# Optimization experiments

Measured on AMD Instinct MI355X. Metric: run time of the kernel, lower is better.

## Reference

```python
import jax, jax.numpy as jnp
import numpy as np


def setup_inputs() -> dict:
    key = jax.random.key(0)
    ks = jax.random.split(key, 5)
    B, S, C = 512, 512, 96
    emissions = jax.random.normal(ks[0], (B, S, C), dtype=jnp.float32)
    tags = jax.random.randint(ks[1], (B, S), 0, C, dtype=jnp.int64)
    masks = jnp.ones((B, S), dtype=bool)
    start_transitions = jax.random.uniform(ks[2], (C,), jnp.float32, -0.1, 0.1)
    end_transitions = jax.random.uniform(ks[3], (C,), jnp.float32, -0.1, 0.1)
    transitions = jax.random.uniform(ks[4], (C, C), jnp.float32, -0.1, 0.1)
    return {
        "emissions": emissions,
        "tags": tags,
        "masks": masks,
        "start_transitions": start_transitions,
        "end_transitions": end_transitions,
        "transitions": transitions,
    }


def _crf_llh(emissions, tags, masks, start_transitions, end_transitions, transitions):
    # to time-major: (S, B, C), (S, B)
    emissions = jnp.swapaxes(emissions, 0, 1)
    tags = jnp.swapaxes(tags, 0, 1)
    masks = jnp.swapaxes(masks, 0, 1)
    S, B, C = emissions.shape
    maskf = masks.astype(emissions.dtype)

    # ---- numerator: score of the gold tag path (fully vectorized over time) ----
    em_scores = jnp.take_along_axis(emissions, tags[:, :, None], axis=2)[:, :, 0]  # (S, B)
    trans_scores = transitions[tags[:-1], tags[1:]]  # (S-1, B)
    score = start_transitions[tags[0]] + em_scores[0]
    score = score + jnp.sum((trans_scores + em_scores[1:]) * maskf[1:], axis=0)
    seq_ends = masks.astype(jnp.int32).sum(axis=0) - 1  # (B,)
    last_tags = tags[seq_ends, jnp.arange(B)]
    numerator = score + end_transitions[last_tags]

    # ---- denominator: forward algorithm (sequential logsumexp recurrence) ----
    alpha0 = start_transitions[None, :] + emissions[0]  # (B, C)

    def step(alpha, inp):
        em_i, m_i = inp  # (B, C), (B,)
        # (B, C_prev, C_next)
        scores = alpha[:, :, None] + transitions[None, :, :] + em_i[:, None, :]
        next_alpha = jax.scipy.special.logsumexp(scores, axis=1)
        alpha = jnp.where(m_i[:, None], next_alpha, alpha)
        return alpha, None

    alpha, _ = jax.lax.scan(step, alpha0, (emissions[1:], masks[1:]))
    denominator = jax.scipy.special.logsumexp(alpha + end_transitions[None, :], axis=1)

    return jnp.mean(numerator - denominator)


def reference(emissions, tags, masks, start_transitions, end_transitions, transitions):
    return _crf_llh(emissions, tags, masks, start_transitions, end_transitions, transitions)
```

## Files before the change

### kernel.cpp

```cpp
#include <hip/hip_runtime.h>
#include <hip/hip_bf16.h>
#include <math.h>


#define BATCH 512
#define SEQ   512
#define NC    96
#define NTHR  128
#define LN2   0.69314718055994531f

typedef __fp16 half2v __attribute__((ext_vector_type(2)));

#define BARRIER() asm volatile("s_waitcnt lgkmcnt(0)\n\ts_barrier" ::: "memory")

#define DPP_STEP_F(v, op, ctrl)                                              \
    v = op(v, __int_as_float(__builtin_amdgcn_update_dpp(                    \
            __float_as_int(v), __float_as_int(v), (ctrl), 0xf, 0xf, false)))

__device__ __forceinline__ float wave_max_all(float v) {
    DPP_STEP_F(v, fmaxf, 0x111);
    DPP_STEP_F(v, fmaxf, 0x112);
    DPP_STEP_F(v, fmaxf, 0x114);
    DPP_STEP_F(v, fmaxf, 0x118);
    DPP_STEP_F(v, fmaxf, 0x142);
    DPP_STEP_F(v, fmaxf, 0x143);
    return __int_as_float(__builtin_amdgcn_readlane(__float_as_int(v), 63));
}
__device__ __forceinline__ float fadd_(float a, float b) { return a + b; }
__device__ __forceinline__ float wave_sum_all(float v) {
    DPP_STEP_F(v, fadd_, 0x111);
    DPP_STEP_F(v, fadd_, 0x112);
    DPP_STEP_F(v, fadd_, 0x114);
    DPP_STEP_F(v, fadd_, 0x118);
    DPP_STEP_F(v, fadd_, 0x142);
    DPP_STEP_F(v, fadd_, 0x143);
    return __int_as_float(__builtin_amdgcn_readlane(__float_as_int(v), 63));
}

__global__ __launch_bounds__(NTHR, 1)
void crf_llh_kernel(const float* __restrict__ em,
                    const int*   __restrict__ tags,
                    const int*   __restrict__ masks,
                    const float* __restrict__ startT,
                    const float* __restrict__ endT,
                    const float* __restrict__ trans,
                    float*       __restrict__ out)
{
    const int b    = blockIdx.x;
    const int tid  = threadIdx.x;
    const int lane = tid & 63;
    const int wid  = tid >> 6;
    const bool active = (tid < NC);
    const int jc = active ? tid : 0;

    __shared__ __align__(16) __fp16 qsh[2][128];
    __shared__ float maxsh[2][2];
    __shared__ float redn[2], redm[2], redd[2];

    const float* em_b    = em    + (size_t)b * SEQ * NC;
    const int*   tags_b  = tags  + b * SEQ;
    const int*   masks_b = masks + b * SEQ;

    half2v ecol[48];
    #pragma unroll
    for (int k = 0; k < 48; ++k) {
        ecol[k] = __builtin_amdgcn_cvt_pkrtz(
            __expf(trans[(2 * k)     * NC + jc]),
            __expf(trans[(2 * k + 1) * NC + jc]));
    }

    const float al0 = startT[jc] + em_b[jc];
    {
        const float wm = wave_max_all(active ? al0 : -1e30f);
        if (lane == 0) maxsh[0][wid] = wm;
    }
    BARRIER();
    const float M0 = fmaxf(maxsh[0][0], maxsh[0][1]);
    float wreg = active ? __expf(al0 - M0) : 0.f;
    qsh[1][tid] = (__fp16)wreg;
    BARRIER();

    int K    = 1;
    int sumk = 0;

    float emA = em_b[1 * NC + jc];
    float emB = em_b[2 * NC + jc];
    float emC = em_b[3 * NC + jc];
    int mkA = masks_b[1], mkB = masks_b[2], mkC = masks_b[3];

    for (int s = 1; s < SEQ; ++s) {
        const int rb = s & 1;
        const int sp = (s + 3 < SEQ) ? (s + 3) : (SEQ - 1);
        const float emN = em_b[sp * NC + jc];
        const int   mkN = masks_b[sp];

        const uint4* q4p = reinterpret_cast<const uint4*>(&qsh[rb][0]);
        uint4 qv[12];
        #pragma unroll
        for (int t = 0; t < 12; ++t) qv[t] = q4p[t];

        float acc[6] = {0.f, 0.f, 0.f, 0.f, 0.f, 0.f};
        #pragma unroll
        for (int t = 0; t < 12; ++t) {
            const half2v qx = __builtin_bit_cast(half2v, qv[t].x);
            const half2v qy = __builtin_bit_cast(half2v, qv[t].y);
            const half2v qz = __builtin_bit_cast(half2v, qv[t].z);
            const half2v qw = __builtin_bit_cast(half2v, qv[t].w);
            acc[(4 * t + 0) % 6] = __builtin_amdgcn_fdot2(qx, ecol[4 * t + 0], acc[(4 * t + 0) % 6], false);
            acc[(4 * t + 1) % 6] = __builtin_amdgcn_fdot2(qy, ecol[4 * t + 1], acc[(4 * t + 1) % 6], false);
            acc[(4 * t + 2) % 6] = __builtin_amdgcn_fdot2(qz, ecol[4 * t + 2], acc[(4 * t + 2) % 6], false);
            acc[(4 * t + 3) % 6] = __builtin_amdgcn_fdot2(qw, ecol[4 * t + 3], acc[(4 * t + 3) % 6], false);
        }
        const float U = ((acc[0] + acc[1]) + (acc[2] + acc[3])) + (acc[4] + acc[5]);

        const float F = __expf(emA);
        float w = ldexpf(U, -(K + 6)) * F;
        if (!active) w = 0.f;
        w = mkA ? w : wreg;
        sumk += mkA ? (K + 6) : 0;
        wreg = w;

        const float wmx = wave_max_all(w);
        if (lane == 0) maxsh[rb][wid] = wmx;
        qsh[rb ^ 1][tid] = (__fp16)w;
        BARRIER();

        const float r = fmaxf(maxsh[rb][0], maxsh[rb][1]);
        K = (int)((__float_as_uint(r) >> 23) & 255u) - 126;

        emA = emB; emB = emC; emC = emN;
        mkA = mkB; mkB = mkC; mkC = mkN;
    }

    const float dv = active ? wreg * __expf(endT[jc]) : 0.f;
    {
        const float ws = wave_sum_all(dv);
        if (lane == 0) redd[wid] = ws;
    }
    __syncthreads();
    const float denom = M0 + (float)sumk * LN2 + __logf(redd[0] + redd[1]);

    float nsum = 0.f, msum = 0.f;
    #pragma unroll
    for (int kk = 0; kk < SEQ / NTHR; ++kk) {
        const int s  = tid + NTHR * kk;
        const int tg = tags_b[s];
        const int mk = masks_b[s];
        msum += mk ? 1.f : 0.f;
        if (s == 0) {
            nsum += startT[tg] + em_b[tg];
        } else if (mk) {
            nsum += trans[tags_b[s - 1] * NC + tg] + em_b[s * NC + tg];
        }
    }
    nsum = wave_sum_all(nsum);
    msum = wave_sum_all(msum);
    if (lane == 0) { redn[wid] = nsum; redm[wid] = msum; }
    __syncthreads();
    if (tid == 0) {
        const float numer = redn[0] + redn[1];
        const int   cnt   = (int)(redm[0] + redm[1]);
        const int   last  = tags_b[cnt - 1];
        atomicAdd(out, (numer + endT[last] - denom) * (1.0f / (float)BATCH));
    }
}

extern "C" void kernel_launch(void* const* d_in, const int* in_sizes, int n_in,
                              void* d_out, int out_size, void* d_ws, size_t ws_size,
                              hipStream_t stream) {
    const float* em     = (const float*)d_in[0];
    const int*   tags   = (const int*)  d_in[1];
    const int*   masks  = (const int*)  d_in[2];
    const float* startT = (const float*)d_in[3];
    const float* endT   = (const float*)d_in[4];
    const float* trans  = (const float*)d_in[5];
    float* out = (float*)d_out;

    (void)hipMemsetAsync(out, 0, sizeof(float), stream);
    crf_llh_kernel<<<BATCH, NTHR, 0, stream>>>(em, tags, masks, startT, endT, trans, out);
}
```

Baseline: 402.9 us.

## Batch 16 sequences per block and run forward recurrence on MFMA

The forward-algorithm recurrence now handles 16 batch rows per block, so each step becomes a 16x96 by 96x96 fp16 matrix product on MFMA instructions instead of per-thread fdot2 loops. A second wave acts as a producer that prefetches emissions, exponentiates them to fp16 and stages them in a 16-slot shared ring, so one barrier covers every four steps. Rescaling uses per-row power-of-two exponents. The numerator moves to a separate kernel. This cuts the grid to 32 blocks, which lowers occupancy, and adds fp16 rounding risk and a second launch.

New measurement: 581.2 us. 44.3% more time.

```diff
diff --git a/kernel.cpp b/kernel.cpp
--- a/kernel.cpp
+++ b/kernel.cpp
@@ -1,15 +1,21 @@
 #include <hip/hip_runtime.h>
-#include <hip/hip_bf16.h>
 #include <math.h>
 
 
 #define BATCH 512
 #define SEQ   512
 #define NC    96
+#define CH    16
+#define NBLK  (BATCH/CH)
 #define NTHR  128
 #define LN2   0.69314718055994531f
+#define FPAT  0x0001000100010001ull
 
 typedef __fp16 half2v __attribute__((ext_vector_type(2)));
+typedef __fp16 half8  __attribute__((ext_vector_type(8)));
+typedef float  f32x4  __attribute__((ext_vector_type(4)));
+typedef unsigned int uint2v __attribute__((ext_vector_type(2)));
+typedef unsigned int uint4v __attribute__((ext_vector_type(4)));
 
 #define BARRIER() asm volatile("s_waitcnt lgkmcnt(0)\n\ts_barrier" ::: "memory")
 
@@ -36,110 +42,311 @@
     DPP_STEP_F(v, fadd_, 0x143);
     return __int_as_float(__builtin_amdgcn_readlane(__float_as_int(v), 63));
 }
+__device__ __forceinline__ float grp16_max(float v) {
+    DPP_STEP_F(v, fmaxf, 0xB1);
+    DPP_STEP_F(v, fmaxf, 0x4E);
+    DPP_STEP_F(v, fmaxf, 0x141);
+    DPP_STEP_F(v, fmaxf, 0x140);
+    return v;
+}
+__device__ __forceinline__ unsigned pk_rtn(float a, float b) {
+    half2v h; h[0] = (__fp16)a; h[1] = (__fp16)b;
+    return __builtin_bit_cast(unsigned, h);
+}
+__device__ __forceinline__ float dot8(half8 a, uint4v b, float c) {
+    uint4v au = __builtin_bit_cast(uint4v, a);
+    c = __builtin_amdgcn_fdot2(__builtin_bit_cast(half2v, au.x), __builtin_bit_cast(half2v, b.x), c, false);
+    c = __builtin_amdgcn_fdot2(__builtin_bit_cast(half2v, au.y), __builtin_bit_cast(half2v, b.y), c, false);
+    c = __builtin_amdgcn_fdot2(__builtin_bit_cast(half2v, au.z), __builtin_bit_cast(half2v, b.z), c, false);
+    c = __builtin_amdgcn_fdot2(__builtin_bit_cast(half2v, au.w), __builtin_bit_cast(half2v, b.w), c, false);
+    return c;
+}
 
 __global__ __launch_bounds__(NTHR, 1)
-void crf_llh_kernel(const float* __restrict__ em,
-                    const int*   __restrict__ tags,
-                    const int*   __restrict__ masks,
-                    const float* __restrict__ startT,
-                    const float* __restrict__ endT,
-                    const float* __restrict__ trans,
-                    float*       __restrict__ out)
+void crf_denom_kernel(const float* __restrict__ em,
+                      const int*   __restrict__ masks,
+                      const float* __restrict__ startT,
+                      const float* __restrict__ endT,
+                      const float* __restrict__ trans,
+                      float*       __restrict__ out)
+{
+    const int tid = threadIdx.x;
+    const int l   = tid & 63;
+    const int w   = tid >> 6;
+    const int c0  = blockIdx.x * CH;
+    const int grp = l >> 4;
+    const int lid = l & 15;
+
+    __shared__ __align__(16) __fp16 Wl[NC * CH];
+    __shared__ __align__(16) __fp16 EMR[16][CH * 104];
+    __shared__ __align__(8)  unsigned short FLG[16][CH];
+    __shared__ __align__(16) __fp16 ENDX[NC];
+    __shared__ int SKC[CH];
+
+    if (w == 0) {
+        float Ms;
+        {
+            float a = startT[l];
+            float b = (l < 32) ? startT[64 + l] : -1e30f;
+            Ms = wave_max_all(fmaxf(a, b));
+        }
+        if (l < 48)
+            ((unsigned*)ENDX)[l] = pk_rtn(__expf(endT[2 * l]), __expf(endT[2 * l + 1]));
+        #pragma unroll
+        for (int t = 0; t < 12; ++t) {
+            const int di = t * 64 + l;
+            const int k  = di >> 3;
+            const float v0 = __expf(startT[k] - Ms);
+            ((unsigned*)Wl)[di] = pk_rtn(v0, v0);
+        }
+        half8 Eb[3][6];
+        #pragma unroll
+        for (int t = 0; t < 3; ++t)
+            #pragma unroll
+            for (int nt = 0; nt < 6; ++nt) {
+                half8 bv;
+                #pragma unroll
+                for (int j = 0; j < 8; ++j)
+                    bv[j] = (__fp16)__expf(trans[(32 * t + grp * 8 + j) * NC + nt * 16 + lid]);
+                Eb[t][nt] = bv;
+            }
+
+        const unsigned wtr = (unsigned)(unsigned long long)Wl + (unsigned)(grp * 256);
+        char* const wpc    = (char*)Wl + lid * 32 + grp * 8;
+        const int   emoff  = lid * 104 + grp * 8;
+
+        half8 ap0{}, ap1{}, ap2{};
+        float m0 = 1.f, m1 = 1.f, m2 = 1.f, m3 = 1.f;
+        float scl0 = 1.f, scl1 = 1.f, scl2 = 1.f, scl3 = 1.f;
+        int   ks0 = 0, ks1 = 0, ks2 = 0, ks3 = 0;
+        int   sk0 = 0, sk1 = 0, sk2 = 0, sk3 = 0;
+
+        #pragma unroll 1
+        for (int s = 1; s <= SEQ - 1; ++s) {
+            if ((s & 3) == 1) BARRIER();
+            const int slotc = (s - 1) & 15;
+            const unsigned long long fqp =
+                *(const unsigned long long*)(&FLG[slotc][grp * 4]);
+            uint2v t0, t1, t2, t3, t4, t5;
+            asm volatile("ds_read_b64_tr_b16 %0, %1"             : "=v"(t0) : "v"(wtr) : "memory");
+            asm volatile("ds_read_b64_tr_b16 %0, %1 offset:128"  : "=v"(t1) : "v"(wtr) : "memory");
+            asm volatile("ds_read_b64_tr_b16 %0, %1 offset:1024" : "=v"(t2) : "v"(wtr) : "memory");
+            asm volatile("ds_read_b64_tr_b16 %0, %1 offset:1152" : "=v"(t3) : "v"(wtr) : "memory");
+            asm volatile("ds_read_b64_tr_b16 %0, %1 offset:2048" : "=v"(t4) : "v"(wtr) : "memory");
+            asm volatile("ds_read_b64_tr_b16 %0, %1 offset:2176" : "=v"(t5) : "v"(wtr) : "memory");
+            const __fp16* emp = &EMR[slotc][0] + emoff;
+            const uint4v e0 = *(const uint4v*)(emp);
+            const uint4v e1 = *(const uint4v*)(emp + 32);
+            const uint4v e2 = *(const uint4v*)(emp + 64);
+            const int allp = __all(fqp == FPAT);
+
+            m0 = grp16_max(m0); m1 = grp16_max(m1);
+            m2 = grp16_max(m2); m3 = grp16_max(m3);
+            const unsigned eb0 = (__float_as_uint(m0) >> 23) & 255u;
+            const unsigned eb1 = (__float_as_uint(m1) >> 23) & 255u;
+            const unsigned eb2 = (__float_as_uint(m2) >> 23) & 255u;
+            const unsigned eb3 = (__float_as_uint(m3) >> 23) & 255u;
+            if (allp) {
+                sk0 += ks0; sk1 += ks1; sk2 += ks2; sk3 += ks3;
+                ks0 = (int)eb0 - 120; ks1 = (int)eb1 - 120;
+                ks2 = (int)eb2 - 120; ks3 = (int)eb3 - 120;
+                scl0 = __uint_as_float((247u - eb0) << 23);
+                scl1 = __uint_as_float((247u - eb1) << 23);
+                scl2 = __uint_as_float((247u - eb2) << 23);
+                scl3 = __uint_as_float((247u - eb3) << 23);
+            } else {
+                if ((unsigned)(fqp      ) & 1u) { sk0 += ks0; ks0 = (int)eb0 - 120; scl0 = __uint_as_float((247u - eb0) << 23); }
+                if ((unsigned)(fqp >> 16) & 1u) { sk1 += ks1; ks1 = (int)eb1 - 120; scl1 = __uint_as_float((247u - eb1) << 23); }
+                if ((unsigned)(fqp >> 32) & 1u) { sk2 += ks2; ks2 = (int)eb2 - 120; scl2 = __uint_as_float((247u - eb2) << 23); }
+                if ((unsigned)(fqp >> 48) & 1u) { sk3 += ks3; ks3 = (int)eb3 - 120; scl3 = __uint_as_float((247u - eb3) << 23); }
+            }
+
+            asm volatile("s_waitcnt lgkmcnt(0)" ::: "memory");
+            __builtin_amdgcn_sched_barrier(0);
+            uint4v u4;
+            u4.x = t0.x; u4.y = t0.y; u4.z = t1.x; u4.w = t1.y;
+            const half8 aw0 = __builtin_bit_cast(half8, u4);
+            u4.x = t2.x; u4.y = t2.y; u4.z = t3.x; u4.w = t3.y;
+            const half8 aw1 = __builtin_bit_cast(half8, u4);
+            u4.x = t4.x; u4.y = t4.y; u4.z = t5.x; u4.w = t5.y;
+            const half8 aw2 = __builtin_bit_cast(half8, u4);
+            const half8 an0 = aw0 * __builtin_bit_cast(half8, e0);
+            const half8 an1 = aw1 * __builtin_bit_cast(half8, e1);
+            const half8 an2 = aw2 * __builtin_bit_cast(half8, e2);
+            if (allp) { ap0 = an0; ap1 = an1; ap2 = an2; }
+            else {
+                const bool fc = (FLG[slotc][lid] != 0);
+                ap0 = fc ? an0 : ap0;
+                ap1 = fc ? an1 : ap1;
+                ap2 = fc ? an2 : ap2;
+            }
+
+            f32x4 acc[6];
+            #pragma unroll
+            for (int nt = 0; nt < 6; ++nt) {
+                const f32x4 z = {0.f, 0.f, 0.f, 0.f};
+                acc[nt] = __builtin_amdgcn_mfma_f32_16x16x32_f16(ap0, Eb[0][nt], z,       0, 0, 0);
+                acc[nt] = __builtin_amdgcn_mfma_f32_16x16x32_f16(ap1, Eb[1][nt], acc[nt], 0, 0, 0);
+                acc[nt] = __builtin_amdgcn_mfma_f32_16x16x32_f16(ap2, Eb[2][nt], acc[nt], 0, 0, 0);
+            }
+
+            float nm0 = -1e30f, nm1 = -1e30f, nm2 = -1e30f, nm3 = -1e30f;
+            #pragma unroll
+            for (int nt = 0; nt < 6; ++nt) {
+                const float u0 = acc[nt][0] * scl0, u1 = acc[nt][1] * scl1;
+                const float u2 = acc[nt][2] * scl2, u3 = acc[nt][3] * scl3;
+                nm0 = fmaxf(nm0, u0); nm1 = fmaxf(nm1, u1);
+                nm2 = fmaxf(nm2, u2); nm3 = fmaxf(nm3, u3);
+                uint2v wv; wv.x = pk_rtn(u0, u1); wv.y = pk_rtn(u2, u3);
+                *(uint2v*)(wpc + 512 * nt) = wv;
+            }
+            m0 = nm0; m1 = nm1; m2 = nm2; m3 = nm3;
+        }
+
+        {
+            const int slotc = (SEQ - 1) & 15;
+            const unsigned long long fqp =
+                *(const unsigned long long*)(&FLG[slotc][grp * 4]);
+            const int allp = __all(fqp == FPAT);
+            if (allp) { sk0 += ks0; sk1 += ks1; sk2 += ks2; sk3 += ks3; }
+            else {
+                if ((unsigned)(fqp      ) & 1u) sk0 += ks0;
+                if ((unsigned)(fqp >> 16) & 1u) sk1 += ks1;
+                if ((unsigned)(fqp >> 32) & 1u) sk2 += ks2;
+                if ((unsigned)(fqp >> 48) & 1u) sk3 += ks3;
+            }
+            uint2v t0, t1, t2, t3, t4, t5;
+            asm volatile("ds_read_b64_tr_b16 %0, %1"             : "=v"(t0) : "v"(wtr) : "memory");
+            asm volatile("ds_read_b64_tr_b16 %0, %1 offset:128"  : "=v"(t1) : "v"(wtr) : "memory");
+            asm volatile("ds_read_b64_tr_b16 %0, %1 offset:1024" : "=v"(t2) : "v"(wtr) : "memory");
+            asm volatile("ds_read_b64_tr_b16 %0, %1 offset:1152" : "=v"(t3) : "v"(wtr) : "memory");
+            asm volatile("ds_read_b64_tr_b16 %0, %1 offset:2048" : "=v"(t4) : "v"(wtr) : "memory");
+            asm volatile("ds_read_b64_tr_b16 %0, %1 offset:2176" : "=v"(t5) : "v"(wtr) : "memory");
+            const __fp16* emp = &EMR[slotc][0] + emoff;
+            const uint4v e0 = *(const uint4v*)(emp);
+            const uint4v e1 = *(const uint4v*)(emp + 32);
+            const uint4v e2 = *(const uint4v*)(emp + 64);
+            asm volatile("s_waitcnt lgkmcnt(0)" ::: "memory");
+            __builtin_amdgcn_sched_barrier(0);
+            uint4v u4;
+            u4.x = t0.x; u4.y = t0.y; u4.z = t1.x; u4.w = t1.y;
+            const half8 aw0 = __builtin_bit_cast(half8, u4);
+            u4.x = t2.x; u4.y = t2.y; u4.z = t3.x; u4.w = t3.y;
+            const half8 aw1 = __builtin_bit_cast(half8, u4);
+            u4.x = t4.x; u4.y = t4.y; u4.z = t5.x; u4.w = t5.y;
+            const half8 aw2 = __builtin_bit_cast(half8, u4);
+            const half8 an0 = aw0 * __builtin_bit_cast(half8, e0);
+            const half8 an1 = aw1 * __builtin_bit_cast(half8, e1);
+            const half8 an2 = aw2 * __builtin_bit_cast(half8, e2);
+            if (allp) { ap0 = an0; ap1 = an1; ap2 = an2; }
+            else {
+                const bool fc = (FLG[slotc][lid] != 0);
+                ap0 = fc ? an0 : ap0;
+                ap1 = fc ? an1 : ap1;
+                ap2 = fc ? an2 : ap2;
+            }
+            const __fp16* ex = ENDX + grp * 8;
+            const uint4v x0 = *(const uint4v*)(ex);
+            const uint4v x1 = *(const uint4v*)(ex + 32);
+            const uint4v x2 = *(const uint4v*)(ex + 64);
+            float dv = dot8(ap2, x2, dot8(ap1, x1, dot8(ap0, x0, 0.f)));
+            dv += __int_as_float(__builtin_amdgcn_ds_swizzle(__float_as_int(dv), 0x401F));
+            dv += __int_as_float(__builtin_amdgcn_ds_bpermute((l ^ 32) << 2, __float_as_int(dv)));
+            if (lid < 4) {
+                int skv = sk0;
+                if (lid == 1) skv = sk1;
+                else if (lid == 2) skv = sk2;
+                else if (lid == 3) skv = sk3;
+                SKC[grp * 4 + lid] = skv;
+            }
+            const int skc = SKC[lid];
+            const float den = Ms + (float)skc * LN2 + __logf(dv);
+            float contrib = (l < 16) ? den : 0.f;
+            contrib = wave_sum_all(contrib);
+            if (tid == 0) atomicAdd(out, -contrib * (1.0f / (float)BATCH));
+        }
+    } else {
+        const int q  = l;
+        const int ch = q >> 2;
+        const int cb = (q & 3) * 24;
+        const float* emc  = em + (size_t)(c0 + ch) * SEQ * NC + cb;
+        const int*   mrow = masks + (size_t)(c0 + ((q < CH) ? q : 0)) * SEQ;
+
+#define STAGE6(SL, V0, V1, V2, V3, V4, V5, FV) do {                           \
+        uint4v* _d = (uint4v*)(&EMR[(SL)][ch * 104 + cb]);                    \
+        uint4v _w0 = { pk_rtn(__expf((V0).x), __expf((V0).y)),                \
+                       pk_rtn(__expf((V0).z), __expf((V0).w)),                \
+                       pk_rtn(__expf((V1).x), __expf((V1).y)),                \
+                       pk_rtn(__expf((V1).z), __expf((V1).w)) };              \
+        uint4v _w1 = { pk_rtn(__expf((V2).x), __expf((V2).y)),                \
+                       pk_rtn(__expf((V2).z), __expf((V2).w)),                \
+                       pk_rtn(__expf((V3).x), __expf((V3).y)),                \
+                       pk_rtn(__expf((V3).z), __expf((V3).w)) };              \
+        uint4v _w2 = { pk_rtn(__expf((V4).x), __expf((V4).y)),                \
+                       pk_rtn(__expf((V4).z), __expf((V4).w)),                \
+                       pk_rtn(__expf((V5).x), __expf((V5).y)) };              \
+        _w2.w = pk_rtn(__expf((V5).z), __expf((V5).w));                       \
+        _d[0] = _w0; _d[1] = _w1; _d[2] = _w2;                                \
+        if (q < CH) FLG[(SL)][q] = (unsigned short)(FV);                      \
+    } while (0)
+
+#define LOAD6(E, V0, V1, V2, V3, V4, V5, FV) do {                             \
+        const float* _p = emc + (size_t)(E) * NC;                             \
+        V0 = *(const float4*)(_p + 0);  V1 = *(const float4*)(_p + 4);        \
+        V2 = *(const float4*)(_p + 8);  V3 = *(const float4*)(_p + 12);       \
+        V4 = *(const float4*)(_p + 16); V5 = *(const float4*)(_p + 20);       \
+        if (q < CH) FV = (mrow[(E)] != 0);                                    \
+    } while (0)
+
+        for (int e = 0; e < 8; ++e) {
+            float4 v0, v1, v2, v3, v4, v5; int fv = 1;
+            LOAD6(e, v0, v1, v2, v3, v4, v5, fv);
+            STAGE6(e, v0, v1, v2, v3, v4, v5, (e == 0) ? 1 : fv);
+        }
+        float4 a0, a1, a2, a3, a4, a5, b0, b1, b2, b3, b4, b5;
+        int fa = 1, fb = 1;
+        LOAD6(8, a0, a1, a2, a3, a4, a5, fa);
+        LOAD6(9, b0, b1, b2, b3, b4, b5, fb);
+
+        #pragma unroll 1
+        for (int s = 1; s <= SEQ - 1; s += 2) {
+            if ((s & 3) == 1) BARRIER();
+            {
+                const int e = s + 7;
+                if (e <= SEQ - 1) STAGE6(e & 15, a0, a1, a2, a3, a4, a5, fa);
+                const int e2 = s + 9;
+                if (e2 <= SEQ - 1) LOAD6(e2, a0, a1, a2, a3, a4, a5, fa);
+            }
+            const int s2 = s + 1;
+            if (s2 <= SEQ - 1) {
+                const int e = s2 + 7;
+                if (e <= SEQ - 1) STAGE6(e & 15, b0, b1, b2, b3, b4, b5, fb);
+                const int e2 = s2 + 9;
+                if (e2 <= SEQ - 1) LOAD6(e2, b0, b1, b2, b3, b4, b5, fb);
+            }
+        }
+#undef STAGE6
+#undef LOAD6
+    }
+}
+
+__global__ __launch_bounds__(NTHR, 1)
+void crf_numer_kernel(const float* __restrict__ em,
+                      const int*   __restrict__ tags,
+                      const int*   __restrict__ masks,
+                      const float* __restrict__ startT,
+                      const float* __restrict__ endT,
+                      const float* __restrict__ trans,
+                      float*       __restrict__ out)
 {
     const int b    = blockIdx.x;
     const int tid  = threadIdx.x;
     const int lane = tid & 63;
     const int wid  = tid >> 6;
-    const bool active = (tid < NC);
-    const int jc = active ? tid : 0;
-
-    __shared__ __align__(16) __fp16 qsh[2][128];
-    __shared__ float maxsh[2][2];
-    __shared__ float redn[2], redm[2], redd[2];
-
+    __shared__ float redn[2], redm[2];
     const float* em_b    = em    + (size_t)b * SEQ * NC;
     const int*   tags_b  = tags  + b * SEQ;
     const int*   masks_b = masks + b * SEQ;
-
-    half2v ecol[48];
-    #pragma unroll
-    for (int k = 0; k < 48; ++k) {
-        ecol[k] = __builtin_amdgcn_cvt_pkrtz(
-            __expf(trans[(2 * k)     * NC + jc]),
-            __expf(trans[(2 * k + 1) * NC + jc]));
-    }
-
-    const float al0 = startT[jc] + em_b[jc];
-    {
-        const float wm = wave_max_all(active ? al0 : -1e30f);
-        if (lane == 0) maxsh[0][wid] = wm;
-    }
-    BARRIER();
-    const float M0 = fmaxf(maxsh[0][0], maxsh[0][1]);
-    float wreg = active ? __expf(al0 - M0) : 0.f;
-    qsh[1][tid] = (__fp16)wreg;
-    BARRIER();
-
-    int K    = 1;
-    int sumk = 0;
-
-    float emA = em_b[1 * NC + jc];
-    float emB = em_b[2 * NC + jc];
-    float emC = em_b[3 * NC + jc];
-    int mkA = masks_b[1], mkB = masks_b[2], mkC = masks_b[3];
-
-    for (int s = 1; s < SEQ; ++s) {
-        const int rb = s & 1;
-        const int sp = (s + 3 < SEQ) ? (s + 3) : (SEQ - 1);
-        const float emN = em_b[sp * NC + jc];
-        const int   mkN = masks_b[sp];
-
-        const uint4* q4p = reinterpret_cast<const uint4*>(&qsh[rb][0]);
-        uint4 qv[12];
-        #pragma unroll
-        for (int t = 0; t < 12; ++t) qv[t] = q4p[t];
-
-        float acc[6] = {0.f, 0.f, 0.f, 0.f, 0.f, 0.f};
-        #pragma unroll
-        for (int t = 0; t < 12; ++t) {
-            const half2v qx = __builtin_bit_cast(half2v, qv[t].x);
-            const half2v qy = __builtin_bit_cast(half2v, qv[t].y);
-            const half2v qz = __builtin_bit_cast(half2v, qv[t].z);
-            const half2v qw = __builtin_bit_cast(half2v, qv[t].w);
-            acc[(4 * t + 0) % 6] = __builtin_amdgcn_fdot2(qx, ecol[4 * t + 0], acc[(4 * t + 0) % 6], false);
-            acc[(4 * t + 1) % 6] = __builtin_amdgcn_fdot2(qy, ecol[4 * t + 1], acc[(4 * t + 1) % 6], false);
-            acc[(4 * t + 2) % 6] = __builtin_amdgcn_fdot2(qz, ecol[4 * t + 2], acc[(4 * t + 2) % 6], false);
-            acc[(4 * t + 3) % 6] = __builtin_amdgcn_fdot2(qw, ecol[4 * t + 3], acc[(4 * t + 3) % 6], false);
-        }
-        const float U = ((acc[0] + acc[1]) + (acc[2] + acc[3])) + (acc[4] + acc[5]);
-
-        const float F = __expf(emA);
-        float w = ldexpf(U, -(K + 6)) * F;
-        if (!active) w = 0.f;
-        w = mkA ? w : wreg;
-        sumk += mkA ? (K + 6) : 0;
-        wreg = w;
-
-        const float wmx = wave_max_all(w);
-        if (lane == 0) maxsh[rb][wid] = wmx;
-        qsh[rb ^ 1][tid] = (__fp16)w;
-        BARRIER();
-
-        const float r = fmaxf(maxsh[rb][0], maxsh[rb][1]);
-        K = (int)((__float_as_uint(r) >> 23) & 255u) - 126;
-
-        emA = emB; emB = emC; emC = emN;
-        mkA = mkB; mkB = mkC; mkC = mkN;
-    }
-
-    const float dv = active ? wreg * __expf(endT[jc]) : 0.f;
-    {
-        const float ws = wave_sum_all(dv);
-        if (lane == 0) redd[wid] = ws;
-    }
-    __syncthreads();
-    const float denom = M0 + (float)sumk * LN2 + __logf(redd[0] + redd[1]);
-
     float nsum = 0.f, msum = 0.f;
     #pragma unroll
     for (int kk = 0; kk < SEQ / NTHR; ++kk) {
@@ -161,7 +368,7 @@
         const float numer = redn[0] + redn[1];
         const int   cnt   = (int)(redm[0] + redm[1]);
         const int   last  = tags_b[cnt - 1];
-        atomicAdd(out, (numer + endT[last] - denom) * (1.0f / (float)BATCH));
+        atomicAdd(out, (numer + endT[last]) * (1.0f / (float)BATCH));
     }
 }
 
@@ -177,5 +384,6 @@
     float* out = (float*)d_out;
 
     (void)hipMemsetAsync(out, 0, sizeof(float), stream);
-    crf_llh_kernel<<<BATCH, NTHR, 0, stream>>>(em, tags, masks, startT, endT, trans, out);
-}
+    crf_denom_kernel<<<NBLK, NTHR, 0, stream>>>(em, masks, startT, endT, trans, out);
+    crf_numer_kernel<<<BATCH, NTHR, 0, stream>>>(em, tags, masks, startT, endT, trans, out);
+}
```

## Batch 16 sequences per block with MFMA recurrence and producer-wave emission staging

Applied to the files above, without the earlier changes.

Each block now handles 16 batch rows instead of one. One wave runs the forward recurrence as 16x16x32 fp16 MFMAs against exp(transitions) held in registers, rescaling with a per-step fp16 max exponent. A second wave streams exp(emissions) into a 16-slot shared ring buffer ahead of the consumer and computes the gold-path numerator. The aim is to replace per-row dot2 work and per-step block reductions with matrix-core throughput and to overlap global loads. The trade-offs are fp16 range and precision risk in the scaling, and only 32 blocks on a large GPU.

Measured after the change: 618.4 us. 1.54x slower.

```diff
diff --git a/kernel.cpp b/kernel.cpp
--- a/kernel.cpp
+++ b/kernel.cpp
@@ -1,15 +1,20 @@
 #include <hip/hip_runtime.h>
-#include <hip/hip_bf16.h>
 #include <math.h>
 
 
 #define BATCH 512
 #define SEQ   512
 #define NC    96
+#define CH    16
+#define NBLK  (BATCH/CH)
 #define NTHR  128
 #define LN2   0.69314718055994531f
 
 typedef __fp16 half2v __attribute__((ext_vector_type(2)));
+typedef __fp16 half8  __attribute__((ext_vector_type(8)));
+typedef float  f32x4  __attribute__((ext_vector_type(4)));
+typedef unsigned int uint2v __attribute__((ext_vector_type(2)));
+typedef unsigned int uint4v __attribute__((ext_vector_type(4)));
 
 #define BARRIER() asm volatile("s_waitcnt lgkmcnt(0)\n\ts_barrier" ::: "memory")
 
@@ -17,15 +22,6 @@
     v = op(v, __int_as_float(__builtin_amdgcn_update_dpp(                    \
             __float_as_int(v), __float_as_int(v), (ctrl), 0xf, 0xf, false)))
 
-__device__ __forceinline__ float wave_max_all(float v) {
-    DPP_STEP_F(v, fmaxf, 0x111);
-    DPP_STEP_F(v, fmaxf, 0x112);
-    DPP_STEP_F(v, fmaxf, 0x114);
-    DPP_STEP_F(v, fmaxf, 0x118);
-    DPP_STEP_F(v, fmaxf, 0x142);
-    DPP_STEP_F(v, fmaxf, 0x143);
-    return __int_as_float(__builtin_amdgcn_readlane(__float_as_int(v), 63));
-}
 __device__ __forceinline__ float fadd_(float a, float b) { return a + b; }
 __device__ __forceinline__ float wave_sum_all(float v) {
     DPP_STEP_F(v, fadd_, 0x111);
@@ -37,131 +33,261 @@
     return __int_as_float(__builtin_amdgcn_readlane(__float_as_int(v), 63));
 }
 
+__device__ __forceinline__ unsigned pkmax(unsigned a, unsigned b) {
+    unsigned d;
+    asm("v_pk_max_f16 %0, %1, %2" : "=v"(d) : "v"(a), "v"(b));
+    return d;
+}
+__device__ __forceinline__ unsigned pk2(float a, float b) {
+    return __builtin_bit_cast(unsigned, __builtin_amdgcn_cvt_pkrtz(a, b));
+}
+__device__ __forceinline__ float dot8(half8 a, uint4v b, float c) {
+    uint4v au = __builtin_bit_cast(uint4v, a);
+    c = __builtin_amdgcn_fdot2(__builtin_bit_cast(half2v, au.x), __builtin_bit_cast(half2v, b.x), c, false);
+    c = __builtin_amdgcn_fdot2(__builtin_bit_cast(half2v, au.y), __builtin_bit_cast(half2v, b.y), c, false);
+    c = __builtin_amdgcn_fdot2(__builtin_bit_cast(half2v, au.z), __builtin_bit_cast(half2v, b.z), c, false);
+    c = __builtin_amdgcn_fdot2(__builtin_bit_cast(half2v, au.w), __builtin_bit_cast(half2v, b.w), c, false);
+    return c;
+}
+
 __global__ __launch_bounds__(NTHR, 1)
-void crf_llh_kernel(const float* __restrict__ em,
-                    const int*   __restrict__ tags,
-                    const int*   __restrict__ masks,
-                    const float* __restrict__ startT,
-                    const float* __restrict__ endT,
-                    const float* __restrict__ trans,
-                    float*       __restrict__ out)
+void crf_fused_kernel(const float* __restrict__ em,
+                      const int*   __restrict__ tags,
+                      const int*   __restrict__ masks,
+                      const float* __restrict__ startT,
+                      const float* __restrict__ endT,
+                      const float* __restrict__ trans,
+                      float*       __restrict__ out)
 {
-    const int b    = blockIdx.x;
-    const int tid  = threadIdx.x;
-    const int lane = tid & 63;
-    const int wid  = tid >> 6;
-    const bool active = (tid < NC);
-    const int jc = active ? tid : 0;
-
-    __shared__ __align__(16) __fp16 qsh[2][128];
-    __shared__ float maxsh[2][2];
-    __shared__ float redn[2], redm[2], redd[2];
-
-    const float* em_b    = em    + (size_t)b * SEQ * NC;
-    const int*   tags_b  = tags  + b * SEQ;
-    const int*   masks_b = masks + b * SEQ;
-
-    half2v ecol[48];
-    #pragma unroll
-    for (int k = 0; k < 48; ++k) {
-        ecol[k] = __builtin_amdgcn_cvt_pkrtz(
-            __expf(trans[(2 * k)     * NC + jc]),
-            __expf(trans[(2 * k + 1) * NC + jc]));
-    }
-
-    const float al0 = startT[jc] + em_b[jc];
-    {
-        const float wm = wave_max_all(active ? al0 : -1e30f);
-        if (lane == 0) maxsh[0][wid] = wm;
-    }
-    BARRIER();
-    const float M0 = fmaxf(maxsh[0][0], maxsh[0][1]);
-    float wreg = active ? __expf(al0 - M0) : 0.f;
-    qsh[1][tid] = (__fp16)wreg;
-    BARRIER();
-
-    int K    = 1;
-    int sumk = 0;
-
-    float emA = em_b[1 * NC + jc];
-    float emB = em_b[2 * NC + jc];
-    float emC = em_b[3 * NC + jc];
-    int mkA = masks_b[1], mkB = masks_b[2], mkC = masks_b[3];
-
-    for (int s = 1; s < SEQ; ++s) {
-        const int rb = s & 1;
-        const int sp = (s + 3 < SEQ) ? (s + 3) : (SEQ - 1);
-        const float emN = em_b[sp * NC + jc];
-        const int   mkN = masks_b[sp];
-
-        const uint4* q4p = reinterpret_cast<const uint4*>(&qsh[rb][0]);
-        uint4 qv[12];
+    const int tid = threadIdx.x;
+    const int l   = tid & 63;
+    const int w   = tid >> 6;
+    const int c0  = blockIdx.x * CH;
+
+    __shared__ __align__(16) __fp16 EMR[16][CH * 104];
+    __shared__ __align__(8)  unsigned short FLG[16][CH];
+
+    if (w == 0) {
+        const int n = l & 15;
+        const int g = l >> 4;
+        const bool hi = (g >= 2);
+        const int addrE = ((32 * (g & 1)) + n) << 2;
+        const int addrO = addrE + (16 << 2);
+        const int addrX32 = (l ^ 32) << 2;
+
+        half8 Ea[6][3];
         #pragma unroll
-        for (int t = 0; t < 12; ++t) qv[t] = q4p[t];
-
-        float acc[6] = {0.f, 0.f, 0.f, 0.f, 0.f, 0.f};
+        for (int r = 0; r < 6; ++r)
+            #pragma unroll
+            for (int c = 0; c < 3; ++c) {
+                half8 v;
+                #pragma unroll
+                for (int e2 = 0; e2 < 8; ++e2)
+                    v[e2] = (__fp16)__expf(trans[(32 * c + 8 * g + e2) * NC + 16 * r + n]);
+                Ea[r][c] = v;
+            }
+
+        BARRIER();
+
+        uint4v Bw[3];
         #pragma unroll
-        for (int t = 0; t < 12; ++t) {
-            const half2v qx = __builtin_bit_cast(half2v, qv[t].x);
-            const half2v qy = __builtin_bit_cast(half2v, qv[t].y);
-            const half2v qz = __builtin_bit_cast(half2v, qv[t].z);
-            const half2v qw = __builtin_bit_cast(half2v, qv[t].w);
-            acc[(4 * t + 0) % 6] = __builtin_amdgcn_fdot2(qx, ecol[4 * t + 0], acc[(4 * t + 0) % 6], false);
-            acc[(4 * t + 1) % 6] = __builtin_amdgcn_fdot2(qy, ecol[4 * t + 1], acc[(4 * t + 1) % 6], false);
-            acc[(4 * t + 2) % 6] = __builtin_amdgcn_fdot2(qz, ecol[4 * t + 2], acc[(4 * t + 2) % 6], false);
-            acc[(4 * t + 3) % 6] = __builtin_amdgcn_fdot2(qw, ecol[4 * t + 3], acc[(4 * t + 3) % 6], false);
-        }
-        const float U = ((acc[0] + acc[1]) + (acc[2] + acc[3])) + (acc[4] + acc[5]);
-
-        const float F = __expf(emA);
-        float w = ldexpf(U, -(K + 6)) * F;
-        if (!active) w = 0.f;
-        w = mkA ? w : wreg;
-        sumk += mkA ? (K + 6) : 0;
-        wreg = w;
-
-        const float wmx = wave_max_all(w);
-        if (lane == 0) maxsh[rb][wid] = wmx;
-        qsh[rb ^ 1][tid] = (__fp16)w;
+        for (int c = 0; c < 3; ++c) {
+            const float4 sa = *(const float4*)(startT + 32 * c + 8 * g);
+            const float4 sb = *(const float4*)(startT + 32 * c + 8 * g + 4);
+            const uint4v E0 = *(const uint4v*)(&EMR[0][n * 104 + 32 * c + 8 * g]);
+            half2v q0 = __builtin_amdgcn_cvt_pkrtz(__expf(sa.x), __expf(sa.y)) * __builtin_bit_cast(half2v, E0.x);
+            half2v q1 = __builtin_amdgcn_cvt_pkrtz(__expf(sa.z), __expf(sa.w)) * __builtin_bit_cast(half2v, E0.y);
+            half2v q2 = __builtin_amdgcn_cvt_pkrtz(__expf(sb.x), __expf(sb.y)) * __builtin_bit_cast(half2v, E0.z);
+            half2v q3 = __builtin_amdgcn_cvt_pkrtz(__expf(sb.z), __expf(sb.w)) * __builtin_bit_cast(half2v, E0.w);
+            Bw[c].x = __builtin_bit_cast(unsigned, q0);
+            Bw[c].y = __builtin_bit_cast(unsigned, q1);
+            Bw[c].z = __builtin_bit_cast(unsigned, q2);
+            Bw[c].w = __builtin_bit_cast(unsigned, q3);
+        }
+
+        int sk = 0;
+
+        #pragma unroll 1
+        for (int s = 1; s < SEQ; ++s) {
+            if ((s & 3) == 1) BARRIER();
+            const int slot = s & 15;
+
+            const __fp16* emrow = &EMR[slot][n * 104 + 4 * g];
+            uint2v emv[6];
+            #pragma unroll
+            for (int r = 0; r < 6; ++r)
+                emv[r] = *(const uint2v*)(emrow + 16 * r);
+            const int flg = FLG[slot][n];
+
+            unsigned t0 = pkmax(Bw[0].x, Bw[0].y), t1 = pkmax(Bw[0].z, Bw[0].w);
+            unsigned t2 = pkmax(Bw[1].x, Bw[1].y), t3 = pkmax(Bw[1].z, Bw[1].w);
+            unsigned t4 = pkmax(Bw[2].x, Bw[2].y), t5 = pkmax(Bw[2].z, Bw[2].w);
+            t0 = pkmax(t0, t1); t2 = pkmax(t2, t3); t4 = pkmax(t4, t5);
+            t0 = pkmax(t0, t2); t0 = pkmax(t0, t4);
+            t0 = pkmax(t0, t0 >> 16);
+            t0 = pkmax(t0, (unsigned)__builtin_amdgcn_ds_swizzle((int)t0, 0x401F));
+            t0 = pkmax(t0, (unsigned)__builtin_amdgcn_ds_bpermute(addrX32, (int)t0));
+            const unsigned eexp = (t0 >> 10) & 31u;
+            const float sclf = __uint_as_float((135u - eexp) << 23);
+            const half2v scl2 = __builtin_amdgcn_cvt_pkrtz(sclf, sclf);
+
+            f32x4 acc[6];
+            const f32x4 z = {0.f, 0.f, 0.f, 0.f};
+            #pragma unroll
+            for (int r = 0; r < 6; ++r)
+                acc[r] = __builtin_amdgcn_mfma_f32_16x16x32_f16(Ea[r][0], __builtin_bit_cast(half8, Bw[0]), z, 0, 0, 0);
+            #pragma unroll
+            for (int r = 0; r < 6; ++r)
+                acc[r] = __builtin_amdgcn_mfma_f32_16x16x32_f16(Ea[r][1], __builtin_bit_cast(half8, Bw[1]), acc[r], 0, 0, 0);
+            #pragma unroll
+            for (int r = 0; r < 6; ++r)
+                acc[r] = __builtin_amdgcn_mfma_f32_16x16x32_f16(Ea[r][2], __builtin_bit_cast(half8, Bw[2]), acc[r], 0, 0, 0);
+
+            unsigned Pw[12];
+            #pragma unroll
+            for (int r = 0; r < 6; ++r) {
+                half2v u01 = __builtin_amdgcn_cvt_pkrtz(acc[r][0], acc[r][1]);
+                half2v u23 = __builtin_amdgcn_cvt_pkrtz(acc[r][2], acc[r][3]);
+                u01 = u01 * (__builtin_bit_cast(half2v, emv[r].x) * scl2);
+                u23 = u23 * (__builtin_bit_cast(half2v, emv[r].y) * scl2);
+                Pw[2 * r]     = __builtin_bit_cast(unsigned, u01);
+                Pw[2 * r + 1] = __builtin_bit_cast(unsigned, u23);
+            }
+
+            #pragma unroll
+            for (int c = 0; c < 3; ++c) {
+                const int p0 = (int)Pw[4 * c],     p1 = (int)Pw[4 * c + 1];
+                const int p2 = (int)Pw[4 * c + 2], p3 = (int)Pw[4 * c + 3];
+                const unsigned a0 = (unsigned)__builtin_amdgcn_ds_bpermute(addrE, p0);
+                const unsigned b0 = (unsigned)__builtin_amdgcn_ds_bpermute(addrE, p2);
+                const unsigned a1 = (unsigned)__builtin_amdgcn_ds_bpermute(addrE, p1);
+                const unsigned b1 = (unsigned)__builtin_amdgcn_ds_bpermute(addrE, p3);
+                const unsigned a2 = (unsigned)__builtin_amdgcn_ds_bpermute(addrO, p0);
+                const unsigned b2 = (unsigned)__builtin_amdgcn_ds_bpermute(addrO, p2);
+                const unsigned a3 = (unsigned)__builtin_amdgcn_ds_bpermute(addrO, p1);
+                const unsigned b3 = (unsigned)__builtin_amdgcn_ds_bpermute(addrO, p3);
+                const unsigned u0 = hi ? b0 : a0;
+                const unsigned u1 = hi ? b1 : a1;
+                const unsigned u2 = hi ? b2 : a2;
+                const unsigned u3 = hi ? b3 : a3;
+                Bw[c].x = flg ? u0 : Bw[c].x;
+                Bw[c].y = flg ? u1 : Bw[c].y;
+                Bw[c].z = flg ? u2 : Bw[c].z;
+                Bw[c].w = flg ? u3 : Bw[c].w;
+            }
+            sk += flg ? ((int)eexp - 8) : 0;
+        }
+
+        float dv = 0.f;
+        #pragma unroll
+        for (int c = 0; c < 3; ++c) {
+            const float4 ea = *(const float4*)(endT + 32 * c + 8 * g);
+            const float4 eb2 = *(const float4*)(endT + 32 * c + 8 * g + 4);
+            uint4v ex;
+            ex.x = pk2(__expf(ea.x), __expf(ea.y));
+            ex.y = pk2(__expf(ea.z), __expf(ea.w));
+            ex.z = pk2(__expf(eb2.x), __expf(eb2.y));
+            ex.w = pk2(__expf(eb2.z), __expf(eb2.w));
+            dv = dot8(__builtin_bit_cast(half8, Bw[c]), ex, dv);
+        }
+        dv += __int_as_float(__builtin_amdgcn_ds_swizzle(__float_as_int(dv), 0x401F));
+        dv += __int_as_float(__builtin_amdgcn_ds_bpermute(addrX32, __float_as_int(dv)));
+        const float den = (float)sk * LN2 + __logf(dv);
+        float contrib = (l < 16) ? den : 0.f;
+        contrib = wave_sum_all(contrib);
+        if (l == 0) atomicAdd(out, -contrib * (1.0f / (float)BATCH));
+    } else {
+        const int q  = l;
+        const int ch = q >> 2;
+        const int cb = (q & 3) * 24;
+        const float* emc  = em + (size_t)(c0 + ch) * SEQ * NC + cb;
+        const int*   mrow = masks + (size_t)(c0 + ch) * SEQ;
+
+#define STAGE6(SL, V0, V1, V2, V3, V4, V5, FV) do {                           \
+        uint4v* _d = (uint4v*)(&EMR[(SL)][ch * 104 + cb]);                    \
+        uint4v _w0 = { pk2(__expf((V0).x), __expf((V0).y)),                   \
+                       pk2(__expf((V0).z), __expf((V0).w)),                   \
+                       pk2(__expf((V1).x), __expf((V1).y)),                   \
+                       pk2(__expf((V1).z), __expf((V1).w)) };                 \
+        uint4v _w1 = { pk2(__expf((V2).x), __expf((V2).y)),                   \
+                       pk2(__expf((V2).z), __expf((V2).w)),                   \
+                       pk2(__expf((V3).x), __expf((V3).y)),                   \
+                       pk2(__expf((V3).z), __expf((V3).w)) };                 \
+        uint4v _w2 = { pk2(__expf((V4).x), __expf((V4).y)),                   \
+                       pk2(__expf((V4).z), __expf((V4).w)),                   \
+                       pk2(__expf((V5).x), __expf((V5).y)) };                 \
+        _w2.w = pk2(__expf((V5).z), __expf((V5).w));                          \
+        _d[0] = _w0; _d[1] = _w1; _d[2] = _w2;                                \
+        if ((q & 3) == 0) FLG[(SL)][ch] = (unsigned short)(FV);               \
+    } while (0)
+
+#define LOAD6(E, V0, V1, V2, V3, V4, V5, FV) do {                             \
+        const float* _p = emc + (size_t)(E) * NC;                             \
+        V0 = *(const float4*)(_p + 0);  V1 = *(const float4*)(_p + 4);        \
+        V2 = *(const float4*)(_p + 8);  V3 = *(const float4*)(_p + 12);       \
+        V4 = *(const float4*)(_p + 16); V5 = *(const float4*)(_p + 20);       \
+        FV = (mrow[(E)] != 0);                                                \
+    } while (0)
+
+        for (int e = 0; e <= 8; ++e) {
+            float4 v0, v1, v2, v3, v4, v5; int fv = 1;
+            LOAD6(e, v0, v1, v2, v3, v4, v5, fv);
+            STAGE6(e, v0, v1, v2, v3, v4, v5, fv);
+        }
+        float4 a0, a1, a2, a3, a4, a5, b0, b1, b2, b3, b4, b5;
+        int fa = 1, fb = 1;
+        LOAD6(9,  a0, a1, a2, a3, a4, a5, fa);
+        LOAD6(10, b0, b1, b2, b3, b4, b5, fb);
+
         BARRIER();
 
-        const float r = fmaxf(maxsh[rb][0], maxsh[rb][1]);
-        K = (int)((__float_as_uint(r) >> 23) & 255u) - 126;
-
-        emA = emB; emB = emC; emC = emN;
-        mkA = mkB; mkB = mkC; mkC = mkN;
-    }
-
-    const float dv = active ? wreg * __expf(endT[jc]) : 0.f;
-    {
-        const float ws = wave_sum_all(dv);
-        if (lane == 0) redd[wid] = ws;
-    }
-    __syncthreads();
-    const float denom = M0 + (float)sumk * LN2 + __logf(redd[0] + redd[1]);
-
-    float nsum = 0.f, msum = 0.f;
-    #pragma unroll
-    for (int kk = 0; kk < SEQ / NTHR; ++kk) {
-        const int s  = tid + NTHR * kk;
-        const int tg = tags_b[s];
-        const int mk = masks_b[s];
-        msum += mk ? 1.f : 0.f;
-        if (s == 0) {
-            nsum += startT[tg] + em_b[tg];
-        } else if (mk) {
-            nsum += trans[tags_b[s - 1] * NC + tg] + em_b[s * NC + tg];
-        }
-    }
-    nsum = wave_sum_all(nsum);
-    msum = wave_sum_all(msum);
-    if (lane == 0) { redn[wid] = nsum; redm[wid] = msum; }
-    __syncthreads();
-    if (tid == 0) {
-        const float numer = redn[0] + redn[1];
-        const int   cnt   = (int)(redm[0] + redm[1]);
-        const int   last  = tags_b[cnt - 1];
-        atomicAdd(out, (numer + endT[last] - denom) * (1.0f / (float)BATCH));
+        #pragma unroll 1
+        for (int s = 1; s < SEQ; s += 2) {
+            if ((s & 3) == 1) BARRIER();
+            {
+                const int e = s + 8;
+                if (e < SEQ) STAGE6(e & 15, a0, a1, a2, a3, a4, a5, fa);
+                const int e2 = s + 10;
+                if (e2 < SEQ) LOAD6(e2, a0, a1, a2, a3, a4, a5, fa);
+            }
+            {
+                const int e = s + 9;
+                if (e < SEQ) STAGE6(e & 15, b0, b1, b2, b3, b4, b5, fb);
+                const int e2 = s + 11;
+                if (e2 < SEQ) LOAD6(e2, b0, b1, b2, b3, b4, b5, fb);
+            }
+        }
+#undef STAGE6
+#undef LOAD6
+
+        const int q4 = l & 3;
+        const int*   tb = tags  + (size_t)(c0 + ch) * SEQ;
+        const float* eb = em    + (size_t)(c0 + ch) * SEQ * NC;
+        float nsum = 0.f, msum = 0.f;
+        #pragma unroll 4
+        for (int kk = 0; kk < SEQ / 4; ++kk) {
+            const int s  = q4 * (SEQ / 4) + kk;
+            const int tg = tb[s];
+            const int mk = mrow[s];
+            msum += mk ? 1.f : 0.f;
+            if (s == 0) {
+                nsum += startT[tg] + eb[tg];
+            } else if (mk) {
+                nsum += trans[tb[s - 1] * NC + tg] + eb[(size_t)s * NC + tg];
+            }
+        }
+        nsum += __int_as_float(__builtin_amdgcn_ds_swizzle(__float_as_int(nsum), 0x041F));
+        nsum += __int_as_float(__builtin_amdgcn_ds_swizzle(__float_as_int(nsum), 0x081F));
+        msum += __int_as_float(__builtin_amdgcn_ds_swizzle(__float_as_int(msum), 0x041F));
+        msum += __int_as_float(__builtin_amdgcn_ds_swizzle(__float_as_int(msum), 0x081F));
+        float contrib = 0.f;
+        if (q4 == 0) {
+            const int cnt  = (int)msum;
+            const int last = tb[cnt - 1];
+            contrib = nsum + endT[last];
+        }
+        contrib = wave_sum_all(contrib);
+        if (l == 0) atomicAdd(out, contrib * (1.0f / (float)BATCH));
     }
 }
 
@@ -177,5 +303,5 @@
     float* out = (float*)d_out;
 
     (void)hipMemsetAsync(out, 0, sizeof(float), stream);
-    crf_llh_kernel<<<BATCH, NTHR, 0, stream>>>(em, tags, masks, startT, endT, trans, out);
-}
+    crf_fused_kernel<<<NBLK, NTHR, 0, stream>>>(em, tags, masks, startT, endT, trans, out);
+}
```
